# Kernel tuning notes

Hardware: AMD Instinct MI355X
Metric: run time of the kernel (lower is better)

## Reference

```python
import math
import jax, jax.numpy as jnp
import numpy as np

NUM_POS_FEATS = 256
TEMPERATURE = 10000.0
NORMALIZE = True
SCALE = 2.0 * math.pi
POSSEG_LEN = 512
EPS = 1e-6

BSZ, L, D = 32, 8192, 256


def setup_inputs() -> dict:
    key = jax.random.key(0)
    kx, km = jax.random.split(key)
    x = jax.random.normal(kx, (BSZ, L, D), dtype=jnp.float32)
    mask = jax.random.randint(km, (BSZ, L), 0, 2, dtype=jnp.int32)
    return {"x": x, "mask": mask}


def _pos_embed(mask):
    """Vectorized segmented-cumsum sinusoidal position embedding.

    Segments of length POSSEG_LEN start at the first valid (mask==1) index of
    each row and tile to the end. Positions before the first valid index, rows
    with no valid positions, and all-zero segments produce x_embed == 0, which
    reproduces the torch default fill (sin(0)=0 at even dims, cos(0)=1 at odd).
    """
    bsz, L = mask.shape
    idx = jnp.arange(L, dtype=jnp.int32)
    valid = mask == 1
    has_valid = jnp.any(valid, axis=1)                       # (B,)
    start = jnp.argmax(valid, axis=1).astype(jnp.int32)      # (B,) first valid idx

    c = jnp.cumsum(mask, axis=1).astype(jnp.float32)         # (B, L) running count
    rel = idx[None, :] - start[:, None]                      # (B, L)
    seg_id = jnp.maximum(rel, 0) // POSSEG_LEN               # (B, L)
    seg_start = start[:, None] + seg_id * POSSEG_LEN         # (B, L)
    seg_end = jnp.minimum(seg_start + POSSEG_LEN, L)         # exclusive end

    # cumsum just before the segment start (0 if segment starts at position 0)
    c_prev = jnp.where(
        seg_start > 0,
        jnp.take_along_axis(c, jnp.maximum(seg_start - 1, 0), axis=1),
        0.0,
    )
    x_embed = c - c_prev                                     # segmented cumsum
    # cumsum value at the last element of each position's segment
    seg_last = jnp.take_along_axis(c, seg_end - 1, axis=1) - c_prev

    in_range = (rel >= 0) & has_valid[:, None]
    x_embed = jnp.where(in_range, x_embed, 0.0)

    if NORMALIZE:
        x_embed = x_embed / (seg_last + EPS) * SCALE

    dim_t = jnp.arange(NUM_POS_FEATS, dtype=jnp.float32)
    dim_t = TEMPERATURE ** (2.0 * jnp.floor(dim_t / 2.0) / NUM_POS_FEATS)

    pos = x_embed[..., None] / dim_t                         # (B, L, F)
    # interleave sin(even dims) and cos(odd dims)
    out = jnp.stack(
        [jnp.sin(pos[..., 0::2]), jnp.cos(pos[..., 1::2])], axis=-1
    ).reshape(bsz, L, NUM_POS_FEATS)
    return out


def reference(x, mask):
    return _pos_embed(mask)
```

## Files before the change

### kernel.cpp

```cpp
#include <hip/hip_runtime.h>
#include <hip/hip_bf16.h>

#define L_LEN   8192
#define SEG     512
#define NFEATS  256
#define SCALE_2PI 6.283185307179586f
#define EPS_REF 1e-6f

#define STEP_LOG2 0.1038102529652301f

__global__ __launch_bounds__(256) void pe_phase1(const int* __restrict__ mask,
                                                 float* __restrict__ xe) {
    constexpr int THREADS = 256;
    constexpr int CHUNK = L_LEN / THREADS;

    __shared__ int c[L_LEN];
    __shared__ int partials[THREADS];
    __shared__ int firstIdx;

    const int t = threadIdx.x;
    const int b = blockIdx.x;
    const int* mrow = mask + (long)b * L_LEN;

    if (t == 0) firstIdx = L_LEN;
    __syncthreads();

    int m[CHUNK];
    const int base = t * CHUNK;
    const int4* mv = (const int4*)(mrow + base);
#pragma unroll
    for (int j = 0; j < CHUNK / 4; ++j) {
        int4 v = mv[j];
        m[4 * j + 0] = v.x; m[4 * j + 1] = v.y;
        m[4 * j + 2] = v.z; m[4 * j + 3] = v.w;
    }

    int s = 0;
    int lf = L_LEN;
#pragma unroll
    for (int j = 0; j < CHUNK; ++j) {
        if (m[j] != 0 && lf == L_LEN) lf = base + j;
        s += m[j];
    }
    partials[t] = s;
    if (lf < L_LEN) atomicMin(&firstIdx, lf);
    __syncthreads();

    for (int off = 1; off < THREADS; off <<= 1) {
        int v = partials[t];
        int add = (t >= off) ? partials[t - off] : 0;
        __syncthreads();
        partials[t] = v + add;
        __syncthreads();
    }

    int run = partials[t] - s;
#pragma unroll
    for (int j = 0; j < CHUNK; ++j) {
        run += m[j];
        c[base + j] = run;
    }
    __syncthreads();

    const int start = firstIdx;
    const bool hv = (start < L_LEN);
    float* xrow = xe + (long)b * L_LEN;

#pragma unroll
    for (int j = 0; j < CHUNK; ++j) {
        const int i = base + j;
        float e = 0.0f;
        const int rel = i - start;
        if (hv && rel >= 0) {
            const int seg_start = start + (rel / SEG) * SEG;
            const int seg_end = min(seg_start + SEG, L_LEN);
            const int cprev = (seg_start > 0) ? c[seg_start - 1] : 0;
            const int ci = c[i];
            const int clast = c[seg_end - 1];
            e = (float)(ci - cprev) / ((float)(clast - cprev) + EPS_REF) * SCALE_2PI;
        }
        xrow[i] = e;
    }
}

__global__ __launch_bounds__(256) void pe_phase2(const float* __restrict__ xe,
                                                 float4* __restrict__ out) {
    const int lane = threadIdx.x & 63;
    const int wave = threadIdx.x >> 6;

    const float inv0 = exp2f(-(float)(2 * lane) * STEP_LOG2);
    const float inv1 = exp2f(-(float)(2 * lane + 1) * STEP_LOG2);

    const int p0 = blockIdx.x * 16 + wave * 4;
#pragma unroll
    for (int j = 0; j < 4; ++j) {
        const int p = p0 + j;
        const float e = xe[p];
        const float t0 = e * inv0;
        const float t1 = e * inv1;
        float s0, c0, s1, c1;
        __sincosf(t0, &s0, &c0);
        __sincosf(t1, &s1, &c1);
        out[(long)p * (NFEATS / 4) + lane] = make_float4(s0, c0, s1, c1);
    }
}

extern "C" void kernel_launch(void* const* d_in, const int* in_sizes, int n_in,
                              void* d_out, int out_size, void* d_ws, size_t ws_size,
                              hipStream_t stream) {
    const int* mask = (const int*)d_in[1];
    float* out = (float*)d_out;
    float* xe = (float*)d_ws;

    const int B = in_sizes[1] / L_LEN;
    const int npos = B * L_LEN;

    pe_phase1<<<dim3(B), dim3(256), 0, stream>>>(mask, xe);
    pe_phase2<<<dim3(npos / 16), dim3(256), 0, stream>>>(xe, (float4*)out);
}
```

Measured before the change: 386.3 us.

## Rewrite segmented cumsum with wave-shuffle scan and use nontemporal output stores

Phase 1 now runs 1024 threads per row and replaces the LDS Hillis-Steele scan and full shared cumsum array with a wave shuffle scan plus per-wave prefix. Per-segment boundary counts and reciprocal scales are precomputed once, so each element needs only a subtract and a multiply, and results are written as float4. Phase 2 loads four embeddings with a single vector load and writes the 256 MB output with nontemporal stores to avoid polluting the cache. The output write dominates the runtime, so the phase 1 changes mostly affect a small kernel.

```diff
diff --git a/kernel.cpp b/kernel.cpp
--- a/kernel.cpp
+++ b/kernel.cpp
@@ -1,5 +1,4 @@
 #include <hip/hip_runtime.h>
-#include <hip/hip_bf16.h>
 
 #define L_LEN   8192
 #define SEG     512
@@ -9,99 +8,126 @@
 
 #define STEP_LOG2 0.1038102529652301f
 
-__global__ __launch_bounds__(256) void pe_phase1(const int* __restrict__ mask,
-                                                 float* __restrict__ xe) {
-    constexpr int THREADS = 256;
+typedef float floatx4 __attribute__((ext_vector_type(4)));
+
+__global__ __launch_bounds__(1024) void pe_phase1(const int* __restrict__ mask,
+                                                  float* __restrict__ xe) {
+    constexpr int THREADS = 1024;
     constexpr int CHUNK = L_LEN / THREADS;
 
-    __shared__ int c[L_LEN];
-    __shared__ int partials[THREADS];
+    __shared__ int waveSum[16];
     __shared__ int firstIdx;
+    __shared__ int cAt[17];
+    __shared__ int cEnd;
+    __shared__ float segCprev[16];
+    __shared__ float segInv[16];
 
     const int t = threadIdx.x;
+    const int lane = t & 63;
+    const int wid = t >> 6;
     const int b = blockIdx.x;
+    const int base = t * CHUNK;
     const int* mrow = mask + (long)b * L_LEN;
 
     if (t == 0) firstIdx = L_LEN;
-    __syncthreads();
 
     int m[CHUNK];
-    const int base = t * CHUNK;
     const int4* mv = (const int4*)(mrow + base);
-#pragma unroll
-    for (int j = 0; j < CHUNK / 4; ++j) {
-        int4 v = mv[j];
-        m[4 * j + 0] = v.x; m[4 * j + 1] = v.y;
-        m[4 * j + 2] = v.z; m[4 * j + 3] = v.w;
-    }
+    int4 v0 = mv[0];
+    int4 v1 = mv[1];
+    m[0] = v0.x; m[1] = v0.y; m[2] = v0.z; m[3] = v0.w;
+    m[4] = v1.x; m[5] = v1.y; m[6] = v1.z; m[7] = v1.w;
 
-    int s = 0;
-    int lf = L_LEN;
+    int s = 0, lf = L_LEN;
 #pragma unroll
     for (int j = 0; j < CHUNK; ++j) {
         if (m[j] != 0 && lf == L_LEN) lf = base + j;
         s += m[j];
     }
-    partials[t] = s;
-    if (lf < L_LEN) atomicMin(&firstIdx, lf);
     __syncthreads();
 
-    for (int off = 1; off < THREADS; off <<= 1) {
-        int v = partials[t];
-        int add = (t >= off) ? partials[t - off] : 0;
-        __syncthreads();
-        partials[t] = v + add;
-        __syncthreads();
+    if (lf < L_LEN) atomicMin(&firstIdx, lf);
+
+    int inc = s;
+#pragma unroll
+    for (int off = 1; off < 64; off <<= 1) {
+        int vv = __shfl_up(inc, off);
+        if (lane >= off) inc += vv;
     }
-
-    int run = partials[t] - s;
-#pragma unroll
-    for (int j = 0; j < CHUNK; ++j) {
-        run += m[j];
-        c[base + j] = run;
-    }
+    if (lane == 63) waveSum[wid] = inc;
     __syncthreads();
 
+    int wavePrefix = 0;
+    for (int w = 0; w < wid; ++w) wavePrefix += waveSum[w];
     const int start = firstIdx;
     const bool hv = (start < L_LEN);
-    float* xrow = xe + (long)b * L_LEN;
+
+    int run = wavePrefix + inc - s;
+    int c[CHUNK];
+#pragma unroll
+    for (int j = 0; j < CHUNK; ++j) { run += m[j]; c[j] = run; }
 
 #pragma unroll
     for (int j = 0; j < CHUNK; ++j) {
         const int i = base + j;
-        float e = 0.0f;
+        const int d = i - start + 1;
+        if (d >= 0 && (d & (SEG - 1)) == 0) {
+            const int q = d >> 9;
+            if (q <= 16) cAt[q] = c[j];
+        }
+        if (i == L_LEN - 1) cEnd = c[j];
+    }
+    __syncthreads();
+
+    if (hv && t < 16) {
+        const int seg_start = start + t * SEG;
+        if (seg_start < L_LEN) {
+            const int cprev = (seg_start == 0) ? 0 : cAt[t];
+            const int seg_end = min(seg_start + SEG, L_LEN);
+            const int clast = (seg_end == L_LEN) ? cEnd : cAt[t + 1];
+            segCprev[t] = (float)cprev;
+            segInv[t] = SCALE_2PI / ((float)(clast - cprev) + EPS_REF);
+        }
+    }
+    __syncthreads();
+
+    float e[CHUNK];
+#pragma unroll
+    for (int j = 0; j < CHUNK; ++j) {
+        const int i = base + j;
         const int rel = i - start;
+        float ev = 0.0f;
         if (hv && rel >= 0) {
-            const int seg_start = start + (rel / SEG) * SEG;
-            const int seg_end = min(seg_start + SEG, L_LEN);
-            const int cprev = (seg_start > 0) ? c[seg_start - 1] : 0;
-            const int ci = c[i];
-            const int clast = c[seg_end - 1];
-            e = (float)(ci - cprev) / ((float)(clast - cprev) + EPS_REF) * SCALE_2PI;
+            const int k = rel >> 9;
+            ev = ((float)c[j] - segCprev[k]) * segInv[k];
         }
-        xrow[i] = e;
+        e[j] = ev;
     }
+    float4* xrow4 = (float4*)(xe + (long)b * L_LEN + base);
+    xrow4[0] = make_float4(e[0], e[1], e[2], e[3]);
+    xrow4[1] = make_float4(e[4], e[5], e[6], e[7]);
 }
 
-__global__ __launch_bounds__(256) void pe_phase2(const float* __restrict__ xe,
-                                                 float4* __restrict__ out) {
+__global__ __launch_bounds__(256) void pe_phase2(const float4* __restrict__ xe4,
+                                                 floatx4* __restrict__ out) {
     const int lane = threadIdx.x & 63;
     const int wave = threadIdx.x >> 6;
 
     const float inv0 = exp2f(-(float)(2 * lane) * STEP_LOG2);
     const float inv1 = exp2f(-(float)(2 * lane + 1) * STEP_LOG2);
 
+    const float4 ev = xe4[blockIdx.x * 4 + wave];
+    const float ea[4] = {ev.x, ev.y, ev.z, ev.w};
+
     const int p0 = blockIdx.x * 16 + wave * 4;
 #pragma unroll
     for (int j = 0; j < 4; ++j) {
-        const int p = p0 + j;
-        const float e = xe[p];
-        const float t0 = e * inv0;
-        const float t1 = e * inv1;
+        const float e = ea[j];
         float s0, c0, s1, c1;
-        __sincosf(t0, &s0, &c0);
-        __sincosf(t1, &s1, &c1);
-        out[(long)p * (NFEATS / 4) + lane] = make_float4(s0, c0, s1, c1);
+        __sincosf(e * inv0, &s0, &c0);
+        __sincosf(e * inv1, &s1, &c1);
+        floatx4 v = {s0, c0, s1, c1};
+        __builtin_nontemporal_store(v, &out[(long)(p0 + j) * (NFEATS / 4) + lane]);
     }
 }
 
@@ -109,12 +135,12 @@
                               void* d_out, int out_size, void* d_ws, size_t ws_size,
                               hipStream_t stream) {
     const int* mask = (const int*)d_in[1];
-    float* out = (float*)d_out;
     float* xe = (float*)d_ws;
 
     const int B = in_sizes[1] / L_LEN;
     const int npos = B * L_LEN;
 
-    pe_phase1<<<dim3(B), dim3(256), 0, stream>>>(mask, xe);
-    pe_phase2<<<dim3(npos / 16), dim3(256), 0, stream>>>(xe, (float4*)out);
+    pe_phase1<<<dim3(B), dim3(1024), 0, stream>>>(mask, xe);
+    pe_phase2<<<dim3(npos / 16), dim3(256), 0, stream>>>((const float4*)xe,
+                                                         (floatx4*)d_out);
 }
```

New measurement: 380.1 us. Within noise of the previous version (-1.6%).
